# Kernel optimization log

Hardware: AMD Instinct MI355X
Metric: run time of the kernel (lower is better)

The kernel has to match this reference:

```python
import jax, jax.numpy as jnp
import numpy as np

DIM = 64  # module-level global `dim` used as the softmax scale


def setup_inputs() -> dict:
    key = jax.random.key(0)
    kq, kk, kv, km = jax.random.split(key, 4)
    B, H, S, d = 4, 16, 2048, DIM
    Q = jax.random.normal(kq, (B, H, S, d), dtype=jnp.float32)
    K = jax.random.normal(kk, (B, H, S, d), dtype=jnp.float32)
    V = jax.random.normal(kv, (B, H, S, d), dtype=jnp.float32)
    attn_mask = jax.random.randint(km, (B, H, S, S), 0, 2).astype(jnp.bool_)
    return {"Q": Q, "K": K, "V": V, "attn_mask": attn_mask}


def reference(Q, K, V, attn_mask):
    scale = 1.0 / np.sqrt(DIM).astype(np.float32)
    # scores: [B, H, S, S]
    scores = jnp.einsum("bhqd,bhkd->bhqk", Q, K) * scale
    # NOTE: original torch code does masked_fill_(attn_mask, 0) — fills with 0, not -inf
    scores = jnp.where(attn_mask, jnp.zeros((), scores.dtype), scores)
    attn = jax.nn.softmax(scores, axis=-1)
    context = jnp.einsum("bhqk,bhkd->bhqd", attn, V)
    return context
```

## Files before the change

### kernel.cpp

```cpp
#include <hip/hip_runtime.h>
#include <hip/hip_bf16.h>

typedef __bf16 bf16;
typedef __attribute__((ext_vector_type(8))) __bf16 bf16x8;
typedef __attribute__((ext_vector_type(4))) __bf16 bf16x4;
typedef __attribute__((ext_vector_type(4))) float f32x4;
typedef __attribute__((ext_vector_type(4))) int i32x4;
typedef __attribute__((ext_vector_type(4))) short s16x4;

constexpr int SLEN = 2048;
constexpr int DH = 64;
constexpr int NBH = 64;
constexpr int NT = SLEN / 64;
constexpr float SCALE_LOG2E = 0.125f * 1.4426950408889634f;

__global__ __launch_bounds__(256) void prep_kv_kernel(
    const float* __restrict__ K, const float* __restrict__ V,
    bf16* __restrict__ Kb, bf16* __restrict__ Vt)
{
    __shared__ float t[64][65];
    const int bh = blockIdx.y;
    const int s0 = blockIdx.x * 64;
    const int tx = threadIdx.x & 63, ty = threadIdx.x >> 6;

    const float* vp = V + ((size_t)bh * SLEN + s0) * DH;
    #pragma unroll
    for (int r = ty; r < 64; r += 4) t[r][tx] = vp[(size_t)r * DH + tx];

    {
        const float* kp = K + ((size_t)bh * SLEN + s0) * DH;
        bf16* kbp = Kb + ((size_t)bh * SLEN + s0) * DH;
        int r = threadIdx.x >> 2, c = (threadIdx.x & 3) * 16;
        const float4* src = (const float4*)(kp + (size_t)r * DH + c);
        float4 a = src[0], b = src[1], c2 = src[2], d = src[3];
        bf16x8 o0, o1;
        o0[0]=(bf16)a.x;  o0[1]=(bf16)a.y;  o0[2]=(bf16)a.z;  o0[3]=(bf16)a.w;
        o0[4]=(bf16)b.x;  o0[5]=(bf16)b.y;  o0[6]=(bf16)b.z;  o0[7]=(bf16)b.w;
        o1[0]=(bf16)c2.x; o1[1]=(bf16)c2.y; o1[2]=(bf16)c2.z; o1[3]=(bf16)c2.w;
        o1[4]=(bf16)d.x;  o1[5]=(bf16)d.y;  o1[6]=(bf16)d.z;  o1[7]=(bf16)d.w;
        *(bf16x8*)(kbp + (size_t)r * DH + c)     = o0;
        *(bf16x8*)(kbp + (size_t)r * DH + c + 8) = o1;
    }

    __syncthreads();
    bf16* op = Vt + (size_t)bh * DH * SLEN + s0;
    #pragma unroll
    for (int r = ty; r < 64; r += 4) op[(size_t)r * SLEN + tx] = (bf16)t[tx][r];
}

__device__ __forceinline__ void gl_lds16(const void* g, void* l) {
    __builtin_amdgcn_global_load_lds(
        (const __attribute__((address_space(1))) void*)g,
        (__attribute__((address_space(3))) void*)l, 16, 0, 0);
}

__device__ __forceinline__ f32x4 pv_mfma(bf16x4 a, bf16x4 b, f32x4 c) {
#if __has_builtin(__builtin_amdgcn_mfma_f32_16x16x16bf16_1k)
    return __builtin_amdgcn_mfma_f32_16x16x16bf16_1k(
        __builtin_bit_cast(s16x4, a), __builtin_bit_cast(s16x4, b), c, 0, 0, 0);
#else
    f32x4 d;
    asm("s_nop 1\n\t"
        "v_mfma_f32_16x16x16_bf16 %0, %1, %2, %3\n\t"
        "s_nop 7"
        : "=v"(d) : "v"(a), "v"(b), "v"(c));
    return d;
#endif
}

__global__ __launch_bounds__(256, 5) void attn_kernel(
    const float* __restrict__ Q, const int* __restrict__ mask,
    const bf16* __restrict__ Kb, const bf16* __restrict__ Vtb,
    float* __restrict__ out)
{
    __shared__ char KT[2][8192];
    __shared__ char VT[2][8192];

    const int h = blockIdx.x;
    const int logical = (h & 7) * 256 + (h >> 3);
    const int bh = logical >> 5;
    const int qbase = (logical & 31) * 64;
    const int tid = threadIdx.x;
    const int w = tid >> 6, l = tid & 63;
    const int lq = l & 15, lg = l >> 4;

    const char* kgb = (const char*)(Kb + (size_t)bh * SLEN * DH);
    const char* vgb = (const char*)(Vtb + (size_t)bh * DH * SLEN);

    const int kv_r = l >> 3;
    const int kv_c = ((l & 7) * 16) ^ (kv_r << 4);

    bf16x8 aq[2];
    {
        const float* qp = Q + ((size_t)bh * SLEN + qbase + w * 16 + lq) * DH + lg * 8;
        #pragma unroll
        for (int t = 0; t < 2; ++t) {
            float4 x = *(const float4*)(qp + t * 32);
            float4 y = *(const float4*)(qp + t * 32 + 4);
            bf16x8 f;
            f[0]=(bf16)x.x; f[1]=(bf16)x.y; f[2]=(bf16)x.z; f[3]=(bf16)x.w;
            f[4]=(bf16)y.x; f[5]=(bf16)y.y; f[6]=(bf16)y.z; f[7]=(bf16)y.w;
            aq[t] = f;
        }
    }

    f32x4 acc[4] = {{0,0,0,0},{0,0,0,0},{0,0,0,0},{0,0,0,0}};
    float dpart = 0.f;
    const int swzk = (lq & 7) << 4;

    const int* mrow = mask + ((size_t)bh * SLEN + qbase + w * 16 + lq) * SLEN;

    auto stage = [&](int t, int buf) {
        const int kb = t * 64;
        #pragma unroll
        for (int q = 0; q < 2; ++q) {
            int r = (w * 2 + q) * 8 + kv_r;
            gl_lds16(kgb + (size_t)(kb + r) * 128 + kv_c, &KT[buf][(w * 2 + q) * 1024]);
            gl_lds16(vgb + (size_t)r * 4096 + (size_t)kb * 2 + kv_c, &VT[buf][(w * 2 + q) * 1024]);
        }
    };
    auto loadmask = [&](int t, i32x4* m) {
        #pragma unroll
        for (int n = 0; n < 4; ++n)
            m[n] = __builtin_nontemporal_load((const i32x4*)(mrow + t * 64 + n * 16 + lg * 4));
    };
    auto body = [&](int cur, const unsigned* pm) {
        bf16x4 p[4];
        #pragma unroll
        for (int n = 0; n < 4; ++n) {
            f32x4 s = {0, 0, 0, 0};
            #pragma unroll
            for (int t = 0; t < 2; ++t) {
                bf16x8 bk = *(const bf16x8*)&KT[cur][(n * 16 + lq) * 128 + ((t * 64 + lg * 16) ^ swzk)];
                s = __builtin_amdgcn_mfma_f32_16x16x32_bf16(bk, aq[t], s, 0, 0, 0);
            }
            #pragma unroll
            for (int i = 0; i < 4; ++i) {
                float pe = exp2f(s[i] * SCALE_LOG2E);
                pe = ((pm[n] >> i) & 1u) ? 1.0f : pe;
                dpart += pe;
                p[n][i] = (bf16)pe;
            }
        }
        #pragma unroll
        for (int nn = 0; nn < 4; ++nn) {
            #pragma unroll
            for (int n = 0; n < 4; ++n) {
                bf16x4 bv = *(const bf16x4*)&VT[cur][(nn * 16 + lq) * 128 + ((n * 32 + lg * 8) ^ swzk)];
                acc[nn] = pv_mfma(p[n], bv, acc[nn]);
            }
        }
    };
    auto tile_sync = [&]() {
        asm volatile("s_waitcnt vmcnt(4) lgkmcnt(0)" ::: "memory");
        __builtin_amdgcn_s_barrier();
        __builtin_amdgcn_sched_barrier(0);
    };

    i32x4 raw[4];
    unsigned pm[4];

    stage(0, 0);
    __builtin_amdgcn_sched_barrier(0);
    loadmask(0, raw);
    tile_sync();

    int cur = 0;
    for (int kt = 0; kt < NT; ++kt) {
        const bool more = (kt + 1) < NT;
        if (more) stage(kt + 1, cur ^ 1);
        __builtin_amdgcn_sched_barrier(0);
        #pragma unroll
        for (int n = 0; n < 4; ++n)
            pm[n] = (raw[n][0] != 0 ? 1u : 0u) | (raw[n][1] != 0 ? 2u : 0u)
                  | (raw[n][2] != 0 ? 4u : 0u) | (raw[n][3] != 0 ? 8u : 0u);
        if (more) loadmask(kt + 1, raw);
        __builtin_amdgcn_sched_barrier(0);
        body(cur, pm);
        if (more) { tile_sync(); cur ^= 1; }
    }

    dpart += __shfl_xor(dpart, 16, 64);
    dpart += __shfl_xor(dpart, 32, 64);
    float dinv = 1.0f / dpart;

    float di[4];
    #pragma unroll
    for (int i = 0; i < 4; ++i) di[i] = __shfl(dinv, lg * 4 + i, 64);

    float* op = out + ((size_t)bh * SLEN + qbase + w * 16) * DH;
    #pragma unroll
    for (int n = 0; n < 4; ++n) {
        #pragma unroll
        for (int i = 0; i < 4; ++i)
            op[(size_t)(lg * 4 + i) * DH + n * 16 + lq] = acc[n][i] * di[i];
    }
}

extern "C" void kernel_launch(void* const* d_in, const int* in_sizes, int n_in,
                              void* d_out, int out_size, void* d_ws, size_t ws_size,
                              hipStream_t stream) {
    const float* Q    = (const float*)d_in[0];
    const float* K    = (const float*)d_in[1];
    const float* V    = (const float*)d_in[2];
    const int*   mask = (const int*)d_in[3];
    float* out = (float*)d_out;

    bf16* Kb  = (bf16*)d_ws;
    bf16* Vtb = Kb + (size_t)NBH * SLEN * DH;

    prep_kv_kernel<<<dim3(SLEN / 64, NBH), 256, 0, stream>>>(K, V, Kb, Vtb);
    attn_kernel<<<2048, 256, 0, stream>>>(Q, mask, Kb, Vtb, out);
}
```

Before: 305.6 us.

## Process two 16-row query groups per wave to reuse staged K/V tiles

After: 807.5 us. 164% more time.

```diff
diff --git a/kernel.cpp b/kernel.cpp
--- a/kernel.cpp
+++ b/kernel.cpp
@@ -68,7 +68,7 @@
 #endif
 }
 
-__global__ __launch_bounds__(256, 5) void attn_kernel(
+__global__ __launch_bounds__(256, 4) void attn_kernel(
     const float* __restrict__ Q, const int* __restrict__ mask,
     const bf16* __restrict__ Kb, const bf16* __restrict__ Vtb,
     float* __restrict__ out)
@@ -77,12 +77,13 @@
     __shared__ char VT[2][8192];
 
     const int h = blockIdx.x;
-    const int logical = (h & 7) * 256 + (h >> 3);
-    const int bh = logical >> 5;
-    const int qbase = (logical & 31) * 64;
+    const int logical = (h & 7) * 128 + (h >> 3);
+    const int bh = logical >> 4;
+    const int qbase = (logical & 15) * 128;
     const int tid = threadIdx.x;
     const int w = tid >> 6, l = tid & 63;
     const int lq = l & 15, lg = l >> 4;
+    const int qrow_w = qbase + w * 32;
 
     const char* kgb = (const char*)(Kb + (size_t)bh * SLEN * DH);
     const char* vgb = (const char*)(Vtb + (size_t)bh * DH * SLEN);
@@ -90,9 +91,10 @@
     const int kv_r = l >> 3;
     const int kv_c = ((l & 7) * 16) ^ (kv_r << 4);
 
-    bf16x8 aq[2];
-    {
-        const float* qp = Q + ((size_t)bh * SLEN + qbase + w * 16 + lq) * DH + lg * 8;
+    bf16x8 aq[2][2];
+    #pragma unroll
+    for (int g = 0; g < 2; ++g) {
+        const float* qp = Q + ((size_t)bh * SLEN + qrow_w + g * 16 + lq) * DH + lg * 8;
         #pragma unroll
         for (int t = 0; t < 2; ++t) {
             float4 x = *(const float4*)(qp + t * 32);
@@ -100,15 +102,17 @@
             bf16x8 f;
             f[0]=(bf16)x.x; f[1]=(bf16)x.y; f[2]=(bf16)x.z; f[3]=(bf16)x.w;
             f[4]=(bf16)y.x; f[5]=(bf16)y.y; f[6]=(bf16)y.z; f[7]=(bf16)y.w;
-            aq[t] = f;
-        }
-    }
-
-    f32x4 acc[4] = {{0,0,0,0},{0,0,0,0},{0,0,0,0},{0,0,0,0}};
-    float dpart = 0.f;
+            aq[g][t] = f;
+        }
+    }
+
+    f32x4 acc[2][4] = {{{0,0,0,0},{0,0,0,0},{0,0,0,0},{0,0,0,0}},
+                       {{0,0,0,0},{0,0,0,0},{0,0,0,0},{0,0,0,0}}};
+    float dpart[2] = {0.f, 0.f};
     const int swzk = (lq & 7) << 4;
 
-    const int* mrow = mask + ((size_t)bh * SLEN + qbase + w * 16 + lq) * SLEN;
+    const int* mrow0 = mask + ((size_t)bh * SLEN + qrow_w + lq) * SLEN;
+    const int* mrow1 = mrow0 + (size_t)16 * SLEN;
 
     auto stage = [&](int t, int buf) {
         const int kb = t * 64;
@@ -119,12 +123,18 @@
             gl_lds16(vgb + (size_t)r * 4096 + (size_t)kb * 2 + kv_c, &VT[buf][(w * 2 + q) * 1024]);
         }
     };
-    auto loadmask = [&](int t, i32x4* m) {
+    auto loadmask = [&](int t, const int* mr, i32x4* m) {
         #pragma unroll
         for (int n = 0; n < 4; ++n)
-            m[n] = __builtin_nontemporal_load((const i32x4*)(mrow + t * 64 + n * 16 + lg * 4));
-    };
-    auto body = [&](int cur, const unsigned* pm) {
+            m[n] = __builtin_nontemporal_load((const i32x4*)(mr + t * 64 + n * 16 + lg * 4));
+    };
+    auto compress = [&](const i32x4* m, unsigned* pm) {
+        #pragma unroll
+        for (int n = 0; n < 4; ++n)
+            pm[n] = (m[n][0] != 0 ? 1u : 0u) | (m[n][1] != 0 ? 2u : 0u)
+                  | (m[n][2] != 0 ? 4u : 0u) | (m[n][3] != 0 ? 8u : 0u);
+    };
+    auto body = [&](int cur, int g, const unsigned* pm) {
         bf16x4 p[4];
         #pragma unroll
         for (int n = 0; n < 4; ++n) {
@@ -132,13 +142,13 @@
             #pragma unroll
             for (int t = 0; t < 2; ++t) {
                 bf16x8 bk = *(const bf16x8*)&KT[cur][(n * 16 + lq) * 128 + ((t * 64 + lg * 16) ^ swzk)];
-                s = __builtin_amdgcn_mfma_f32_16x16x32_bf16(bk, aq[t], s, 0, 0, 0);
+                s = __builtin_amdgcn_mfma_f32_16x16x32_bf16(bk, aq[g][t], s, 0, 0, 0);
             }
             #pragma unroll
             for (int i = 0; i < 4; ++i) {
                 float pe = exp2f(s[i] * SCALE_LOG2E);
                 pe = ((pm[n] >> i) & 1u) ? 1.0f : pe;
-                dpart += pe;
+                dpart[g] += pe;
                 p[n][i] = (bf16)pe;
             }
         }
@@ -147,7 +157,7 @@
             #pragma unroll
             for (int n = 0; n < 4; ++n) {
                 bf16x4 bv = *(const bf16x4*)&VT[cur][(nn * 16 + lq) * 128 + ((n * 32 + lg * 8) ^ swzk)];
-                acc[nn] = pv_mfma(p[n], bv, acc[nn]);
+                acc[g][nn] = pv_mfma(p[n], bv, acc[g][nn]);
             }
         }
     };
@@ -158,42 +168,52 @@
     };
 
     i32x4 raw[4];
-    unsigned pm[4];
+    unsigned pm0[4], pm1[4];
 
     stage(0, 0);
     __builtin_amdgcn_sched_barrier(0);
-    loadmask(0, raw);
+    loadmask(0, mrow0, raw);
     tile_sync();
+    compress(raw, pm0);
+    loadmask(0, mrow1, raw);
+    __builtin_amdgcn_sched_barrier(0);
 
     int cur = 0;
     for (int kt = 0; kt < NT; ++kt) {
         const bool more = (kt + 1) < NT;
         if (more) stage(kt + 1, cur ^ 1);
         __builtin_amdgcn_sched_barrier(0);
-        #pragma unroll
-        for (int n = 0; n < 4; ++n)
-            pm[n] = (raw[n][0] != 0 ? 1u : 0u) | (raw[n][1] != 0 ? 2u : 0u)
-                  | (raw[n][2] != 0 ? 4u : 0u) | (raw[n][3] != 0 ? 8u : 0u);
-        if (more) loadmask(kt + 1, raw);
-        __builtin_amdgcn_sched_barrier(0);
-        body(cur, pm);
+        compress(raw, pm1);
+        if (more) loadmask(kt + 1, mrow0, raw);
+        __builtin_amdgcn_sched_barrier(0);
+        body(cur, 0, pm0);
+        __builtin_amdgcn_sched_barrier(0);
+        if (more) {
+            compress(raw, pm0);
+            loadmask(kt + 1, mrow1, raw);
+        }
+        __builtin_amdgcn_sched_barrier(0);
+        body(cur, 1, pm1);
         if (more) { tile_sync(); cur ^= 1; }
     }
 
-    dpart += __shfl_xor(dpart, 16, 64);
-    dpart += __shfl_xor(dpart, 32, 64);
-    float dinv = 1.0f / dpart;
-
-    float di[4];
-    #pragma unroll
-    for (int i = 0; i < 4; ++i) di[i] = __shfl(dinv, lg * 4 + i, 64);
-
-    float* op = out + ((size_t)bh * SLEN + qbase + w * 16) * DH;
-    #pragma unroll
-    for (int n = 0; n < 4; ++n) {
-        #pragma unroll
-        for (int i = 0; i < 4; ++i)
-            op[(size_t)(lg * 4 + i) * DH + n * 16 + lq] = acc[n][i] * di[i];
+    #pragma unroll
+    for (int g = 0; g < 2; ++g) {
+        float d = dpart[g];
+        d += __shfl_xor(d, 16, 64);
+        d += __shfl_xor(d, 32, 64);
+        float dinv = 1.0f / d;
+        float di[4];
+        #pragma unroll
+        for (int i = 0; i < 4; ++i) di[i] = __shfl(dinv, lg * 4 + i, 64);
+
+        float* op = out + ((size_t)bh * SLEN + qrow_w + g * 16) * DH;
+        #pragma unroll
+        for (int n = 0; n < 4; ++n) {
+            #pragma unroll
+            for (int i = 0; i < 4; ++i)
+                op[(size_t)(lg * 4 + i) * DH + n * 16 + lq] = acc[g][n][i] * di[i];
+        }
     }
 }
 
@@ -210,5 +230,5 @@
     bf16* Vtb = Kb + (size_t)NBH * SLEN * DH;
 
     prep_kv_kernel<<<dim3(SLEN / 64, NBH), 256, 0, stream>>>(K, V, Kb, Vtb);
-    attn_kernel<<<2048, 256, 0, stream>>>(Q, mask, Kb, Vtb, out);
-}
+    attn_kernel<<<1024, 256, 0, stream>>>(Q, mask, Kb, Vtb, out);
+}
```

## Coalesce mask loads row-wise and redistribute bits to MFMA layout via ballot

Applied to the files above, without the earlier changes.

After: 300.8 us, median of 2. About the same (-1.6%).

```diff
diff --git a/kernel.cpp b/kernel.cpp
--- a/kernel.cpp
+++ b/kernel.cpp
@@ -7,6 +7,7 @@
 typedef __attribute__((ext_vector_type(4))) float f32x4;
 typedef __attribute__((ext_vector_type(4))) int i32x4;
 typedef __attribute__((ext_vector_type(4))) short s16x4;
+typedef unsigned long long u64;
 
 constexpr int SLEN = 2048;
 constexpr int DH = 64;
@@ -108,7 +109,8 @@
     float dpart = 0.f;
     const int swzk = (lq & 7) << 4;
 
-    const int* mrow = mask + ((size_t)bh * SLEN + qbase + w * 16 + lq) * SLEN;
+    const int* mrowc = mask + ((size_t)bh * SLEN + qbase + w * 16 + (l >> 4)) * SLEN
+                            + (l & 15) * 4;
 
     auto stage = [&](int t, int buf) {
         const int kb = t * 64;
@@ -121,10 +123,27 @@
     };
     auto loadmask = [&](int t, i32x4* m) {
         #pragma unroll
-        for (int n = 0; n < 4; ++n)
-            m[n] = __builtin_nontemporal_load((const i32x4*)(mrow + t * 64 + n * 16 + lg * 4));
-    };
-    auto body = [&](int cur, const unsigned* pm) {
+        for (int j = 0; j < 4; ++j)
+            m[j] = __builtin_nontemporal_load(
+                (const i32x4*)(mrowc + (size_t)j * 4 * SLEN + t * 64));
+    };
+    const int jsel = lq >> 2;
+    const int shb = (lq & 3) * 16 + lg;
+    auto extract = [&](const i32x4* m) -> unsigned {
+        unsigned pmall = 0;
+        #pragma unroll
+        for (int i = 0; i < 4; ++i) {
+            u64 b0 = __ballot(m[0][i] != 0);
+            u64 b1 = __ballot(m[1][i] != 0);
+            u64 b2 = __ballot(m[2][i] != 0);
+            u64 b3 = __ballot(m[3][i] != 0);
+            u64 b = jsel == 0 ? b0 : jsel == 1 ? b1 : jsel == 2 ? b2 : b3;
+            unsigned lo = (unsigned)(b >> shb) & 0x1111u;
+            pmall |= lo << i;
+        }
+        return pmall;
+    };
+    auto body = [&](int cur, unsigned pmall) {
         bf16x4 p[4];
         #pragma unroll
         for (int n = 0; n < 4; ++n) {
@@ -137,7 +156,7 @@
             #pragma unroll
             for (int i = 0; i < 4; ++i) {
                 float pe = exp2f(s[i] * SCALE_LOG2E);
-                pe = ((pm[n] >> i) & 1u) ? 1.0f : pe;
+                pe = ((pmall >> (n * 4 + i)) & 1u) ? 1.0f : pe;
                 dpart += pe;
                 p[n][i] = (bf16)pe;
             }
@@ -158,7 +177,6 @@
     };
 
     i32x4 raw[4];
-    unsigned pm[4];
 
     stage(0, 0);
     __builtin_amdgcn_sched_barrier(0);
@@ -170,13 +188,10 @@
         const bool more = (kt + 1) < NT;
         if (more) stage(kt + 1, cur ^ 1);
         __builtin_amdgcn_sched_barrier(0);
-        #pragma unroll
-        for (int n = 0; n < 4; ++n)
-            pm[n] = (raw[n][0] != 0 ? 1u : 0u) | (raw[n][1] != 0 ? 2u : 0u)
-                  | (raw[n][2] != 0 ? 4u : 0u) | (raw[n][3] != 0 ? 8u : 0u);
+        unsigned pmall = extract(raw);
         if (more) loadmask(kt + 1, raw);
         __builtin_amdgcn_sched_barrier(0);
-        body(cur, pm);
+        body(cur, pmall);
         if (more) { tile_sync(); cur ^= 1; }
     }
 
```
